# Performance work log

Measured on AMD Instinct MI355X. Metric: run time of the kernel, lower is better.

## Reference

```python
import jax, jax.numpy as jnp
import numpy as np

E, M, K, N = 32, 1024, 512, 512

def setup_inputs() -> dict:
    key = jax.random.key(0)
    k1, k2, k3 = jax.random.split(key, 3)
    A = jax.random.normal(k1, (E, M, K), dtype=jnp.float32)
    B = jax.random.normal(k2, (E, N, K), dtype=jnp.float32)
    expert_num_tokens = jax.random.randint(k3, (E,), 0, M + 1, dtype=jnp.int32)
    return {"A": A, "B": B, "expert_num_tokens": expert_num_tokens}

def reference(A, B, expert_num_tokens):
    # Per-expert GEMM: C[e] = A[e] @ B[e].T  -> [E, M, N]
    C = jnp.einsum('emk,enk->emn', A, B)
    # Rows m >= expert_num_tokens[e] are never computed/stored by the kernel;
    # zero them in the reference output.
    row_valid = jnp.arange(A.shape[1])[None, :] < expert_num_tokens[:, None]  # [E, M]
    return jnp.where(row_valid[:, :, None], C, jnp.zeros((), C.dtype))
```

## Files before the change

kernel.cpp:

```cpp
#include <hip/hip_runtime.h>
#include <hip/hip_bf16.h>

#define NE 32
#define MM 1024
#define KK 512
#define NN 512
#define BM 256
#define BN 256
#define BK 32

typedef __attribute__((ext_vector_type(8))) short bf16x8;
typedef __attribute__((ext_vector_type(4))) float floatx4;

__device__ __forceinline__ short f2bf(float f) {
  union { __hip_bfloat16 b; short s; } u;
  u.b = __float2bfloat16(f);
  return u.s;
}
__device__ __forceinline__ bf16x8 pack8(float4 a, float4 b) {
  return (bf16x8){ f2bf(a.x), f2bf(a.y), f2bf(a.z), f2bf(a.w),
                   f2bf(b.x), f2bf(b.y), f2bf(b.z), f2bf(b.w) };
}

extern "C" __global__ __launch_bounds__(512, 2)
void expert_gemm(const float* __restrict__ A, const float* __restrict__ B,
                 const int* __restrict__ cnts, float* __restrict__ C)
{
  const int b    = blockIdx.x;
  const int tid  = threadIdx.x;
  const int xcd  = b & 7;
  const int slot = b >> 3;

  int e = -1, mt = 0, nt = 0, zfill = 0;
  int base = 0;
#pragma unroll
  for (int i = 0; i < 4; ++i) {
    int ei = xcd + (i << 3);
    int vt = (cnts[ei] + 255) >> 8;
    int tot = vt + 4;
    if (e < 0 && slot < base + tot) {
      int r = slot - base;
      int g = vt << 1;
      e = ei;
      if (r < g) { mt = r >> 1; nt = r & 1; }
      else       { zfill = 1; mt = vt + (r - g); }
    }
    base += tot;
  }
  if (e < 0) return;

  if (zfill) {
    float* Ce = C + ((size_t)e * MM + mt * BM) * NN;
    float4 zf = make_float4(0.f, 0.f, 0.f, 0.f);
#pragma unroll
    for (int q = 0; q < 64; ++q) {
      int fidx = q * 512 + tid;
      int r = fidx >> 7, c = (fidx & 127) << 2;
      *(float4*)(Ce + (size_t)r * NN + c) = zf;
    }
    return;
  }

  const int m0 = mt * BM, n0 = nt * BN;
  const int cnt = cnts[e];
  const float* Ae = A + ((size_t)e * MM + m0) * KK;
  const float* Be = B + ((size_t)e * NN + n0) * KK;
  float* Ce = C + ((size_t)e * MM + m0) * NN + n0;

  __shared__ __align__(16) short lA[2][BM * BK];
  __shared__ __align__(16) short lB[2][BN * BK];

  const int wave = tid >> 6, lane = tid & 63;
  const int wm = (wave >> 2) * 128, wn = (wave & 3) * 64;
  const int fr = lane & 15, kh = lane >> 4;

  const int row0 = tid >> 2, seg = tid & 3;
  const int wu0 = (row0 << 2) + (seg ^ (row0 & 3));
  const int wu1 = ((row0 + 128) << 2) + (seg ^ (row0 & 3));

  floatx4 acc4[8][4] = {};

  float4 ca[4], cb[4], na_[4], nb_[4];

#define ISSUE(pa, pb, KT) do {                                        \
    int colf = (KT) + (seg << 3);                                     \
    pa[0] = *(const float4*)(Ae + (size_t)row0 * KK + colf);          \
    pa[1] = *(const float4*)(Ae + (size_t)row0 * KK + colf + 4);      \
    pa[2] = *(const float4*)(Ae + (size_t)(row0+128) * KK + colf);    \
    pa[3] = *(const float4*)(Ae + (size_t)(row0+128) * KK + colf+4);  \
    pb[0] = *(const float4*)(Be + (size_t)row0 * KK + colf);          \
    pb[1] = *(const float4*)(Be + (size_t)row0 * KK + colf + 4);      \
    pb[2] = *(const float4*)(Be + (size_t)(row0+128) * KK + colf);    \
    pb[3] = *(const float4*)(Be + (size_t)(row0+128) * KK + colf+4);  \
  } while (0)

  ISSUE(ca, cb, 0);

#pragma unroll
  for (int kt = 0; kt < KK; kt += BK) {
    const int cur = (kt >> 5) & 1;
    if (kt + BK < KK) ISSUE(na_, nb_, kt + BK);

    *(bf16x8*)(lA[cur] + (wu0 << 3)) = pack8(ca[0], ca[1]);
    *(bf16x8*)(lA[cur] + (wu1 << 3)) = pack8(ca[2], ca[3]);
    *(bf16x8*)(lB[cur] + (wu0 << 3)) = pack8(cb[0], cb[1]);
    *(bf16x8*)(lB[cur] + (wu1 << 3)) = pack8(cb[2], cb[3]);

    asm volatile("s_waitcnt lgkmcnt(0)" ::: "memory");
    __builtin_amdgcn_s_barrier();
    __builtin_amdgcn_sched_barrier(0);

    bf16x8 bfv[4];
#pragma unroll
    for (int j = 0; j < 4; ++j) {
      int rB = wn + (j << 4) + fr;
      bfv[j] = *(const bf16x8*)(lB[cur] + (((rB << 2) + (kh ^ (rB & 3))) << 3));
    }
    __builtin_amdgcn_s_setprio(1);
#pragma unroll
    for (int i = 0; i < 8; ++i) {
      int rA = wm + (i << 4) + fr;
      bf16x8 af = *(const bf16x8*)(lA[cur] + (((rA << 2) + (kh ^ (rA & 3))) << 3));
#pragma unroll
      for (int j = 0; j < 4; ++j)
        acc4[i][j] = __builtin_amdgcn_mfma_f32_16x16x32_bf16(af, bfv[j], acc4[i][j], 0, 0, 0);
    }
    __builtin_amdgcn_s_setprio(0);

#pragma unroll
    for (int q = 0; q < 4; ++q) { ca[q] = na_[q]; cb[q] = nb_[q]; }
  }
#undef ISSUE

  const int rbase = (lane >> 4) << 2;
#pragma unroll
  for (int i = 0; i < 8; ++i) {
#pragma unroll
    for (int r = 0; r < 4; ++r) {
      int row = wm + (i << 4) + rbase + r;
      bool valid = (m0 + row) < cnt;
#pragma unroll
      for (int j = 0; j < 4; ++j) {
        int col = wn + (j << 4) + fr;
        Ce[(size_t)row * NN + col] = valid ? acc4[i][j][r] : 0.0f;
      }
    }
  }
}

extern "C" void kernel_launch(void* const* d_in, const int* in_sizes, int n_in,
                              void* d_out, int out_size, void* d_ws, size_t ws_size,
                              hipStream_t stream) {
  const float* A    = (const float*)d_in[0];
  const float* B    = (const float*)d_in[1];
  const int*   cnts = (const int*)d_in[2];
  float*       C    = (float*)d_out;

  hipLaunchKernelGGL(expert_gemm, dim3(256), dim3(512), 0, stream, A, B, cnts, C);
}
```

Before: 149.2 us.

## Stream fp32 tiles directly into LDS with global_load_lds, convert at fragment read

Replaces the register-staged load → bf16 pack → LDS store path with direct global-to-LDS DMA (global_load_lds, 16 bytes per lane) of the raw fp32 tiles. The bf16 conversion moves to the LDS fragment reads, using an XOR swizzle over 8 float4 units per row. The goal is to free VGPRs and drop the ds_write traffic, which lets prefetch overlap through vmcnt waits. In exchange LDS usage doubles (fp32 rather than bf16, 128KB per block), which likely blocks the 2-blocks-per-CU occupancy. Every wave also re-converts shared fragments, and a second barrier is added per iteration.

```diff
diff --git a/kernel.cpp b/kernel.cpp
--- a/kernel.cpp
+++ b/kernel.cpp
@@ -8,6 +8,7 @@
 #define BM 256
 #define BN 256
 #define BK 32
+#define KKB 2048
 
 typedef __attribute__((ext_vector_type(8))) short bf16x8;
 typedef __attribute__((ext_vector_type(4))) float floatx4;
@@ -21,6 +22,10 @@
   return (bf16x8){ f2bf(a.x), f2bf(a.y), f2bf(a.z), f2bf(a.w),
                    f2bf(b.x), f2bf(b.y), f2bf(b.z), f2bf(b.w) };
 }
+
+#define GLDS(g, l) __builtin_amdgcn_global_load_lds(                      \
+    (const __attribute__((address_space(1))) void*)(g),                   \
+    (__attribute__((address_space(3))) void*)(l), 16, 0, 0)
 
 extern "C" __global__ __launch_bounds__(512, 2)
 void expert_gemm(const float* __restrict__ A, const float* __restrict__ B,
@@ -67,70 +72,80 @@
   const float* Be = B + ((size_t)e * NN + n0) * KK;
   float* Ce = C + ((size_t)e * MM + m0) * NN + n0;
 
-  __shared__ __align__(16) short lA[2][BM * BK];
-  __shared__ __align__(16) short lB[2][BN * BK];
+  __shared__ __align__(16) float sA[2][BM * BK];
+  __shared__ __align__(16) float sB[2][BN * BK];
 
   const int wave = tid >> 6, lane = tid & 63;
   const int wm = (wave >> 2) * 128, wn = (wave & 3) * 64;
   const int fr = lane & 15, kh = lane >> 4;
 
-  const int row0 = tid >> 2, seg = tid & 3;
-  const int wu0 = (row0 << 2) + (seg ^ (row0 & 3));
-  const int wu1 = ((row0 + 128) << 2) + (seg ^ (row0 & 3));
+  const int lr = lane >> 3;
+  const int lu = (lane & 7) ^ lr;
+  const size_t rowb = (size_t)lr * KKB + (size_t)lu * 16;
+  const char* gA = (const char*)Ae;
+  const char* gB = (const char*)Be;
+
+#define STAGE(bufi, KT) do {                                               \
+    _Pragma("unroll")                                                      \
+    for (int q = 0; q < 4; ++q) {                                          \
+      int grp = (wave << 2) + q;                                           \
+      GLDS(gA + (size_t)(grp << 3) * KKB + rowb + (size_t)(KT) * 4,        \
+           &sA[bufi][grp << 8]);                                           \
+      GLDS(gB + (size_t)(grp << 3) * KKB + rowb + (size_t)(KT) * 4,        \
+           &sB[bufi][grp << 8]);                                           \
+    }                                                                      \
+  } while (0)
 
   floatx4 acc4[8][4] = {};
 
-  float4 ca[4], cb[4], na_[4], nb_[4];
-
-#define ISSUE(pa, pb, KT) do {                                        \
-    int colf = (KT) + (seg << 3);                                     \
-    pa[0] = *(const float4*)(Ae + (size_t)row0 * KK + colf);          \
-    pa[1] = *(const float4*)(Ae + (size_t)row0 * KK + colf + 4);      \
-    pa[2] = *(const float4*)(Ae + (size_t)(row0+128) * KK + colf);    \
-    pa[3] = *(const float4*)(Ae + (size_t)(row0+128) * KK + colf+4);  \
-    pb[0] = *(const float4*)(Be + (size_t)row0 * KK + colf);          \
-    pb[1] = *(const float4*)(Be + (size_t)row0 * KK + colf + 4);      \
-    pb[2] = *(const float4*)(Be + (size_t)(row0+128) * KK + colf);    \
-    pb[3] = *(const float4*)(Be + (size_t)(row0+128) * KK + colf+4);  \
-  } while (0)
-
-  ISSUE(ca, cb, 0);
+  STAGE(0, 0);
 
 #pragma unroll
   for (int kt = 0; kt < KK; kt += BK) {
     const int cur = (kt >> 5) & 1;
-    if (kt + BK < KK) ISSUE(na_, nb_, kt + BK);
 
-    *(bf16x8*)(lA[cur] + (wu0 << 3)) = pack8(ca[0], ca[1]);
-    *(bf16x8*)(lA[cur] + (wu1 << 3)) = pack8(ca[2], ca[3]);
-    *(bf16x8*)(lB[cur] + (wu0 << 3)) = pack8(cb[0], cb[1]);
-    *(bf16x8*)(lB[cur] + (wu1 << 3)) = pack8(cb[2], cb[3]);
-
-    asm volatile("s_waitcnt lgkmcnt(0)" ::: "memory");
+    if (kt + BK < KK) {
+      STAGE(cur ^ 1, kt + BK);
+      asm volatile("s_waitcnt vmcnt(8)" ::: "memory");
+    } else {
+      asm volatile("s_waitcnt vmcnt(0)" ::: "memory");
+    }
     __builtin_amdgcn_s_barrier();
     __builtin_amdgcn_sched_barrier(0);
+
+    const char* bufA = (const char*)sA[cur];
+    const char* bufB = (const char*)sB[cur];
 
     bf16x8 bfv[4];
 #pragma unroll
     for (int j = 0; j < 4; ++j) {
       int rB = wn + (j << 4) + fr;
-      bfv[j] = *(const bf16x8*)(lB[cur] + (((rB << 2) + (kh ^ (rB & 3))) << 3));
+      const char* rb = bufB + rB * 128;
+      float4 f0 = *(const float4*)(rb + ((((kh << 1)    ) ^ (rB & 7)) << 4));
+      float4 f1 = *(const float4*)(rb + ((((kh << 1) | 1) ^ (rB & 7)) << 4));
+      bfv[j] = pack8(f0, f1);
     }
     __builtin_amdgcn_s_setprio(1);
 #pragma unroll
     for (int i = 0; i < 8; ++i) {
       int rA = wm + (i << 4) + fr;
-      bf16x8 af = *(const bf16x8*)(lA[cur] + (((rA << 2) + (kh ^ (rA & 3))) << 3));
+      const char* rb = bufA + rA * 128;
+      float4 f0 = *(const float4*)(rb + ((((kh << 1)    ) ^ (rA & 7)) << 4));
+      float4 f1 = *(const float4*)(rb + ((((kh << 1) | 1) ^ (rA & 7)) << 4));
+      bf16x8 af = pack8(f0, f1);
 #pragma unroll
       for (int j = 0; j < 4; ++j)
         acc4[i][j] = __builtin_amdgcn_mfma_f32_16x16x32_bf16(af, bfv[j], acc4[i][j], 0, 0, 0);
     }
     __builtin_amdgcn_s_setprio(0);
 
-#pragma unroll
-    for (int q = 0; q < 4; ++q) { ca[q] = na_[q]; cb[q] = nb_[q]; }
+    if (kt + BK < KK) {
+      __builtin_amdgcn_sched_barrier(0);
+      __builtin_amdgcn_s_barrier();
+      __builtin_amdgcn_sched_barrier(0);
+    }
   }
-#undef ISSUE
+#undef STAGE
 
   const int rbase = (lane >> 4) << 2;
 #pragma unroll
```

After: 163.2 us. 1.09x slower.
